# Performance work log

Hardware: AMD Instinct MI355X
Metric: run time of the kernel (lower is better)

The kernel has to match this reference:

```python
import jax, jax.numpy as jnp
import numpy as np

N = 400000
IN, H, F, S, OUT = 64, 256, 128, 16, 5


def setup_inputs() -> dict:
    key = jax.random.key(0)
    ks = jax.random.split(key, 20)
    def lin(k, fan_in, fan_out):
        bound = 1.0 / np.sqrt(fan_in)
        kw, kb = jax.random.split(k)
        W = jax.random.uniform(kw, (fan_in, fan_out), jnp.float32, -bound, bound)
        b = jax.random.uniform(kb, (fan_out,), jnp.float32, -bound, bound)
        return W, b
    pw1, pb1 = lin(ks[0], IN, H)
    pw2, pb2 = lin(ks[1], H, H)
    pw3, pb3 = lin(ks[2], H, F)
    rw1, rb1 = lin(ks[3], F, H)
    rw2, rb2 = lin(ks[4], H, H)
    rw3, rb3 = lin(ks[5], H, F)
    w1, b1 = lin(ks[6], F + S, H)
    w2, b2 = lin(ks[7], H, H)
    w3, b3 = lin(ks[8], H, OUT)
    x = jax.random.normal(ks[9], (N, IN), jnp.float32)
    x_static = jax.random.normal(ks[10], (S,), jnp.float32)
    return {
        "x": x, "x_static": x_static,
        "pw1": pw1, "pb1": pb1, "pw2": pw2, "pb2": pb2, "pw3": pw3, "pb3": pb3,
        "rw1": rw1, "rb1": rb1, "rw2": rw2, "rb2": rb2, "rw3": rw3, "rb3": rb3,
        "w1": w1, "b1": b1, "w2": w2, "b2": b2, "w3": w3, "b3": b3,
    }


def reference(x, x_static, pw1, pb1, pw2, pb2, pw3, pb3,
              rw1, rb1, rw2, rb2, rw3, rb3, w1, b1, w2, b2, w3, b3):
    # phi network applied to every row, then sum-pool (DeepSets).
    # Batched matmuls replace the original Python per-row loop; the per-row
    # bias of the final phi Linear is summed N times, matching the loop.
    h = jax.nn.relu(x @ pw1 + pb1)              # [N, H]
    h = jax.nn.relu(h @ pw2 + pb2)              # [N, H]
    phi = h @ pw3 + pb3                          # [N, F]
    fp = jnp.sum(phi, axis=0)                    # [F]
    # rho network
    r = jax.nn.relu(fp @ rw1 + rb1)
    r = jax.nn.relu(r @ rw2 + rb2)
    r = r @ rw3 + rb3                            # [F]
    out = jnp.concatenate([r, x_static], axis=0)  # [F + S]
    out = jax.nn.relu(out @ w1 + b1)
    out = jax.nn.relu(out @ w2 + b2)
    return out @ w3 + b3                          # [OUT]
```

## Files before the change

kernel.cpp:

```cpp
#include <hip/hip_runtime.h>


typedef unsigned short u16;
typedef _Float16 f16x8 __attribute__((ext_vector_type(8)));
typedef _Float16 f16x4v __attribute__((ext_vector_type(4)));
typedef float f32x4 __attribute__((ext_vector_type(4)));
typedef int i32x4 __attribute__((ext_vector_type(4)));

#define NBLK 256

#define OPW3 0
#define ORW1 32768
#define ORW2 65536
#define ORW3 131072
#define OHW1 163840
#define OHW2 200704
#define OHW3 266240
#define NTW  267520

__global__ void prep_kernel(const float* __restrict__ pw1, const float* __restrict__ pw2,
                            _Float16* __restrict__ w1f, _Float16* __restrict__ w2f,
                            float* __restrict__ gsum, _Float16* __restrict__ tw,
                            const float* __restrict__ pw3, const float* __restrict__ rw1,
                            const float* __restrict__ rw2, const float* __restrict__ rw3,
                            const float* __restrict__ hw1, const float* __restrict__ hw2,
                            const float* __restrict__ hw3) {
    int idx = blockIdx.x * blockDim.x + threadIdx.x;
    if (idx < 256) gsum[idx] = 0.f;
    if (idx < 16384) {
        int j = idx & 7, l = (idx >> 3) & 63, ks = (idx >> 9) & 1, ct = idx >> 10;
        int k = 32 * ks + 8 * (l >> 4) + j;
        int col = 16 * ct + (l & 15);
        w1f[idx] = (_Float16)pw1[k * 256 + col];
    } else {
        int o = idx - 16384;
        int j = o & 7, l = (o >> 3) & 63, ks = (o >> 9) & 7, ct = o >> 12;
        int k = 32 * ks + 8 * (l >> 4) + j;
        int col = 16 * ct + (l & 15);
        w2f[o] = (_Float16)pw2[k * 256 + col];
    }
    if (idx < NTW / 4) {
        int r = idx * 4;
        const float* src;
        if (r < ORW1)      src = pw3 + r;
        else if (r < ORW2) src = rw1 + (r - ORW1);
        else if (r < ORW3) src = rw2 + (r - ORW2);
        else if (r < OHW1) src = rw3 + (r - ORW3);
        else if (r < OHW2) src = hw1 + (r - OHW1);
        else if (r < OHW3) src = hw2 + (r - OHW2);
        else               src = hw3 + (r - OHW3);
        float4 v = *(const float4*)src;
        uint2 o;
        o.x = __builtin_bit_cast(unsigned, __builtin_amdgcn_cvt_pkrtz(v.x, v.y));
        o.y = __builtin_bit_cast(unsigned, __builtin_amdgcn_cvt_pkrtz(v.z, v.w));
        *(uint2*)(tw + r) = o;
    }
}

__device__ __forceinline__ void pin_reg(f16x8& v) {
    i32x4 t = __builtin_bit_cast(i32x4, v);
    asm volatile("" : "+v"(t));
    v = __builtin_bit_cast(f16x8, t);
}
__device__ __forceinline__ unsigned pk(float a, float b) {
    return __builtin_bit_cast(unsigned, __builtin_amdgcn_cvt_pkrtz(a, b));
}

__global__ __attribute__((amdgpu_flat_work_group_size(512, 512), amdgpu_waves_per_eu(2, 2)))
void phi_kernel(
    const float* __restrict__ x,
    const float* __restrict__ pb1, const float* __restrict__ pb2,
    const _Float16* __restrict__ w1g, const _Float16* __restrict__ w2g,
    float* __restrict__ gsum, int ntiles) {
    __shared__ __align__(16) u16 xs[2][64 * 64];
    __shared__ __align__(16) u16 h1s[2][64 * 256];

    const int tid = threadIdx.x;
    const int l = tid & 63;
    const int w = tid >> 6;
    const int fr = l & 15;
    const int fg = l >> 4;
    const int wb = w * 32;

    f16x8 w1r[2][2];
#pragma unroll
    for (int ct = 0; ct < 2; ++ct)
#pragma unroll
        for (int ks = 0; ks < 2; ++ks) {
            int ctg = 2 * w + ct;
            w1r[ct][ks] = *(const f16x8*)(w1g + (((ctg << 1) + ks) << 9) + (l << 3));
        }
    f16x8 w2r[2][8];
#pragma unroll
    for (int ct = 0; ct < 2; ++ct)
#pragma unroll
        for (int ks = 0; ks < 8; ++ks) {
            int ctg = 2 * w + ct;
            w2r[ct][ks] = *(const f16x8*)(w2g + (((ctg << 3) + ks) << 9) + (l << 3));
        }
#pragma unroll
    for (int ct = 0; ct < 2; ++ct) {
#pragma unroll
        for (int ks = 0; ks < 2; ++ks) pin_reg(w1r[ct][ks]);
#pragma unroll
        for (int ks = 0; ks < 8; ++ks) pin_reg(w2r[ct][ks]);
    }
    f32x4 b1v[2], b2v[2];
#pragma unroll
    for (int ct = 0; ct < 2; ++ct) {
        int c0 = wb + ct * 16 + fg * 4;
        b1v[ct] = *(const f32x4*)(pb1 + c0);
        b2v[ct] = *(const f32x4*)(pb2 + c0);
    }

    float psum[2][4] = {{0.f, 0.f, 0.f, 0.f}, {0.f, 0.f, 0.f, 0.f}};

    const int t0 = blockIdx.x;
    {
        const float4* xg = (const float4*)(x + (size_t)t0 * 4096);
#pragma unroll
        for (int i = 0; i < 2; ++i) {
            int f4 = tid + i * 512;
            float4 v = xg[f4];
            int row = f4 >> 4, c4 = f4 & 15;
            uint2 o;
            o.x = pk(v.x, v.y);
            o.y = pk(v.z, v.w);
            int byte = (row * 128 + c4 * 8) ^ ((row & 7) << 4);
            *(uint2*)((char*)xs[0] + byte) = o;
        }
    }
    float4 pf0, pf1;
    {
        int tn = (t0 + NBLK < ntiles) ? t0 + NBLK : 0;
        const float4* xg = (const float4*)(x + (size_t)tn * 4096);
        pf0 = xg[tid];
        pf1 = xg[tid + 512];
    }
    __syncthreads();

    int buf = 0, hb = 0;
    for (int t = t0; t < ntiles; t += NBLK) {
#pragma unroll
        for (int i = 0; i < 2; ++i) {
            float4 v = i ? pf1 : pf0;
            int f4 = tid + i * 512;
            int row = f4 >> 4, c4 = f4 & 15;
            uint2 o;
            o.x = pk(v.x, v.y);
            o.y = pk(v.z, v.w);
            int byte = (row * 128 + c4 * 8) ^ ((row & 7) << 4);
            *(uint2*)((char*)xs[buf ^ 1] + byte) = o;
        }
        {
            int tn = (t + 2 * NBLK < ntiles) ? t + 2 * NBLK : 0;
            const float4* xg = (const float4*)(x + (size_t)tn * 4096);
            pf0 = xg[tid];
            pf1 = xg[tid + 512];
        }

        {
            f32x4 acc[2][4] = {};
#pragma unroll
            for (int ks = 0; ks < 2; ++ks) {
                f16x8 bd[4];
#pragma unroll
                for (int rt = 0; rt < 4; ++rt) {
                    int row = (rt << 4) + fr;
                    int byte = ((row << 7) + (ks << 6) + (fg << 4)) ^ ((row & 7) << 4);
                    bd[rt] = *(const f16x8*)((char*)xs[buf] + byte);
                }
#pragma unroll
                for (int ct = 0; ct < 2; ++ct)
#pragma unroll
                    for (int rt = 0; rt < 4; ++rt)
                        acc[ct][rt] = __builtin_amdgcn_mfma_f32_16x16x32_f16(w1r[ct][ks], bd[rt], acc[ct][rt], 0, 0, 0);
            }
#pragma unroll
            for (int ct = 0; ct < 2; ++ct) {
                int c0 = wb + ct * 16 + fg * 4;
#pragma unroll
                for (int rt = 0; rt < 4; ++rt) {
                    int rown = (rt << 4) + fr;
                    uint2 o;
                    o.x = pk(fmaxf(acc[ct][rt][0] + b1v[ct][0], 0.f),
                             fmaxf(acc[ct][rt][1] + b1v[ct][1], 0.f));
                    o.y = pk(fmaxf(acc[ct][rt][2] + b1v[ct][2], 0.f),
                             fmaxf(acc[ct][rt][3] + b1v[ct][3], 0.f));
                    int byte = ((rown << 9) + (c0 << 1)) ^ ((rown & 15) << 4);
                    *(uint2*)((char*)h1s[hb] + byte) = o;
                }
            }
        }
        __syncthreads();

        {
            f32x4 acc2[2][4] = {};
#pragma unroll
            for (int ks = 0; ks < 8; ++ks) {
                f16x8 bd[4];
#pragma unroll
                for (int rt = 0; rt < 4; ++rt) {
                    int row = (rt << 4) + fr;
                    int byte = ((row << 9) + (ks << 6) + (fg << 4)) ^ ((row & 15) << 4);
                    bd[rt] = *(const f16x8*)((char*)h1s[hb] + byte);
                }
#pragma unroll
                for (int ct = 0; ct < 2; ++ct)
#pragma unroll
                    for (int rt = 0; rt < 4; ++rt)
                        acc2[ct][rt] = __builtin_amdgcn_mfma_f32_16x16x32_f16(w2r[ct][ks], bd[rt], acc2[ct][rt], 0, 0, 0);
            }
#pragma unroll
            for (int ct = 0; ct < 2; ++ct)
#pragma unroll
                for (int r = 0; r < 4; ++r) {
                    float v = 0.f;
#pragma unroll
                    for (int rt = 0; rt < 4; ++rt)
                        v += fmaxf(acc2[ct][rt][r] + b2v[ct][r], 0.f);
                    psum[ct][r] += v;
                }
        }
        buf ^= 1;
        hb ^= 1;
    }

#pragma unroll
    for (int ct = 0; ct < 2; ++ct)
#pragma unroll
        for (int r = 0; r < 4; ++r) {
            float v = psum[ct][r];
            v += __shfl_xor(v, 1, 64);
            v += __shfl_xor(v, 2, 64);
            v += __shfl_xor(v, 4, 64);
            v += __shfl_xor(v, 8, 64);
            if (fr == 0) atomicAdd(&gsum[wb + ct * 16 + fg * 4 + r], v);
        }
}

#define LAYER_V4(IN, OUT, OFF, INEXPR, BIASEXPR, OUTARR, DORELU, KQ, KR)       \
    {                                                                          \
        int cg = t & ((OUT) / 4 - 1), q = t / ((OUT) / 4);                     \
        float4 s = make_float4(0.f, 0.f, 0.f, 0.f);                            \
        int i0 = q * (KR);                                                     \
        for (int i = i0; i < i0 + (KR); ++i) {                                 \
            f16x4v wv = *(const f16x4v*)(tw + (OFF) + i * (OUT) + 4 * cg);     \
            float xv = INEXPR;                                                 \
            s.x += xv * (float)wv[0]; s.y += xv * (float)wv[1];                \
            s.z += xv * (float)wv[2]; s.w += xv * (float)wv[3];                \
        }                                                                      \
        *(float4*)&part[q * (OUT) + 4 * cg] = s;                               \
    }                                                                          \
    __syncthreads();                                                           \
    if (t < (OUT)) {                                                           \
        float s = BIASEXPR;                                                    \
        for (int q = 0; q < (KQ); ++q) s += part[q * (OUT) + t];               \
        OUTARR[t] = (DORELU) ? fmaxf(s, 0.f) : s;                              \
    }                                                                          \
    __syncthreads();

__global__ __launch_bounds__(1024) void tail_kernel(
    const float* __restrict__ gsum, const float* __restrict__ xst,
    const _Float16* __restrict__ tw,
    const float* __restrict__ pb3, const float* __restrict__ rb1,
    const float* __restrict__ rb2, const float* __restrict__ rb3,
    const float* __restrict__ hb1, const float* __restrict__ hb2,
    const float* __restrict__ hb3,
    float* __restrict__ out, float nf) {
    __shared__ float fp[128], r1[256], r2[256], tc[144], t1[256], t2[256];
    __shared__ __align__(16) float part[4096];
    const int t = threadIdx.x;

    LAYER_V4(256, 128, OPW3, gsum[i], nf * pb3[t], fp, 0, 32, 8)
    LAYER_V4(128, 256, ORW1, fp[i], rb1[t], r1, 1, 16, 8)
    LAYER_V4(256, 256, ORW2, r1[i], rb2[t], r2, 1, 16, 16)
    LAYER_V4(256, 128, ORW3, r2[i], rb3[t], tc, 0, 32, 8)
    if (t >= 128 && t < 144) tc[t] = xst[t - 128];
    __syncthreads();
    LAYER_V4(144, 256, OHW1, tc[i], hb1[t], t1, 1, 16, 9)
    LAYER_V4(256, 256, OHW2, t1[i], hb2[t], t2, 1, 16, 16)
    {
        int j = t & 255, q = t >> 8, b = 64 * q;
        if (j < 5) {
            float s0 = 0.f, s1 = 0.f;
#pragma unroll
            for (int i = 0; i < 64; i += 2) {
                s0 += t2[b + i]     * (float)tw[OHW3 + (b + i) * 5 + j];
                s1 += t2[b + i + 1] * (float)tw[OHW3 + (b + i + 1) * 5 + j];
            }
            part[q * 8 + j] = s0 + s1;
        }
    }
    __syncthreads();
    if (t < 5) {
        float s = hb3[t];
        for (int q = 0; q < 4; ++q) s += part[q * 8 + t];
        out[t] = s;
    }
}

extern "C" void kernel_launch(void* const* d_in, const int* in_sizes, int n_in,
                              void* d_out, int out_size, void* d_ws, size_t ws_size,
                              hipStream_t stream) {
    (void)n_in; (void)out_size; (void)ws_size;
    const float* x   = (const float*)d_in[0];
    const float* xst = (const float*)d_in[1];
    const float* pw1 = (const float*)d_in[2];
    const float* pb1 = (const float*)d_in[3];
    const float* pw2 = (const float*)d_in[4];
    const float* pb2 = (const float*)d_in[5];
    const float* pw3 = (const float*)d_in[6];
    const float* pb3 = (const float*)d_in[7];
    const float* rw1 = (const float*)d_in[8];
    const float* rb1 = (const float*)d_in[9];
    const float* rw2 = (const float*)d_in[10];
    const float* rb2 = (const float*)d_in[11];
    const float* rw3 = (const float*)d_in[12];
    const float* rb3 = (const float*)d_in[13];
    const float* w1  = (const float*)d_in[14];
    const float* b1  = (const float*)d_in[15];
    const float* w2  = (const float*)d_in[16];
    const float* b2  = (const float*)d_in[17];
    const float* w3  = (const float*)d_in[18];
    const float* b3  = (const float*)d_in[19];
    float* out = (float*)d_out;

    int n = in_sizes[0] / 64;
    int ntiles = n >> 6;

    char* ws = (char*)d_ws;
    float* gsum = (float*)ws;
    _Float16* w1f = (_Float16*)(ws + 2048);
    _Float16* w2f = (_Float16*)(ws + 2048 + 32768);
    _Float16* tw  = (_Float16*)(ws + 2048 + 32768 + 131072);

    prep_kernel<<<160, 512, 0, stream>>>(pw1, pw2, w1f, w2f, gsum, tw,
                                         pw3, rw1, rw2, rw3, w1, w2, w3);
    phi_kernel<<<NBLK, 512, 0, stream>>>(x, pb1, pb2, w1f, w2f, gsum, ntiles);
    tail_kernel<<<1, 1024, 0, stream>>>(gsum, xst, tw, pb3, rb1, rb2, rb3,
                                        b1, b2, b3, out, (float)n);
}
```

Before: 102.1 us.

## Fuse tail MLP into phi kernel via last-block atomic counter

Removes the separate single-block tail kernel launch by having each phi block increment a global counter after its atomic accumulation. The last block to finish runs the rho and head MLP layers itself, reusing the h1s shared buffer as scratch with 512 threads instead of 1024. This saves one kernel launch and its gap, at the cost of thread fences, an extra atomic per block, and a tail computed by half as many threads.

New measurement: 127.4 us. 1.25x slower.

```diff
diff --git a/kernel.cpp b/kernel.cpp
--- a/kernel.cpp
+++ b/kernel.cpp
@@ -26,7 +26,7 @@
                             const float* __restrict__ hw1, const float* __restrict__ hw2,
                             const float* __restrict__ hw3) {
     int idx = blockIdx.x * blockDim.x + threadIdx.x;
-    if (idx < 256) gsum[idx] = 0.f;
+    if (idx < 260) gsum[idx] = 0.f;
     if (idx < 16384) {
         int j = idx & 7, l = (idx >> 3) & 63, ks = (idx >> 9) & 1, ct = idx >> 10;
         int k = 32 * ks + 8 * (l >> 4) + j;
@@ -66,180 +66,7 @@
     return __builtin_bit_cast(unsigned, __builtin_amdgcn_cvt_pkrtz(a, b));
 }
 
-__global__ __attribute__((amdgpu_flat_work_group_size(512, 512), amdgpu_waves_per_eu(2, 2)))
-void phi_kernel(
-    const float* __restrict__ x,
-    const float* __restrict__ pb1, const float* __restrict__ pb2,
-    const _Float16* __restrict__ w1g, const _Float16* __restrict__ w2g,
-    float* __restrict__ gsum, int ntiles) {
-    __shared__ __align__(16) u16 xs[2][64 * 64];
-    __shared__ __align__(16) u16 h1s[2][64 * 256];
-
-    const int tid = threadIdx.x;
-    const int l = tid & 63;
-    const int w = tid >> 6;
-    const int fr = l & 15;
-    const int fg = l >> 4;
-    const int wb = w * 32;
-
-    f16x8 w1r[2][2];
-#pragma unroll
-    for (int ct = 0; ct < 2; ++ct)
-#pragma unroll
-        for (int ks = 0; ks < 2; ++ks) {
-            int ctg = 2 * w + ct;
-            w1r[ct][ks] = *(const f16x8*)(w1g + (((ctg << 1) + ks) << 9) + (l << 3));
-        }
-    f16x8 w2r[2][8];
-#pragma unroll
-    for (int ct = 0; ct < 2; ++ct)
-#pragma unroll
-        for (int ks = 0; ks < 8; ++ks) {
-            int ctg = 2 * w + ct;
-            w2r[ct][ks] = *(const f16x8*)(w2g + (((ctg << 3) + ks) << 9) + (l << 3));
-        }
-#pragma unroll
-    for (int ct = 0; ct < 2; ++ct) {
-#pragma unroll
-        for (int ks = 0; ks < 2; ++ks) pin_reg(w1r[ct][ks]);
-#pragma unroll
-        for (int ks = 0; ks < 8; ++ks) pin_reg(w2r[ct][ks]);
-    }
-    f32x4 b1v[2], b2v[2];
-#pragma unroll
-    for (int ct = 0; ct < 2; ++ct) {
-        int c0 = wb + ct * 16 + fg * 4;
-        b1v[ct] = *(const f32x4*)(pb1 + c0);
-        b2v[ct] = *(const f32x4*)(pb2 + c0);
-    }
-
-    float psum[2][4] = {{0.f, 0.f, 0.f, 0.f}, {0.f, 0.f, 0.f, 0.f}};
-
-    const int t0 = blockIdx.x;
-    {
-        const float4* xg = (const float4*)(x + (size_t)t0 * 4096);
-#pragma unroll
-        for (int i = 0; i < 2; ++i) {
-            int f4 = tid + i * 512;
-            float4 v = xg[f4];
-            int row = f4 >> 4, c4 = f4 & 15;
-            uint2 o;
-            o.x = pk(v.x, v.y);
-            o.y = pk(v.z, v.w);
-            int byte = (row * 128 + c4 * 8) ^ ((row & 7) << 4);
-            *(uint2*)((char*)xs[0] + byte) = o;
-        }
-    }
-    float4 pf0, pf1;
-    {
-        int tn = (t0 + NBLK < ntiles) ? t0 + NBLK : 0;
-        const float4* xg = (const float4*)(x + (size_t)tn * 4096);
-        pf0 = xg[tid];
-        pf1 = xg[tid + 512];
-    }
-    __syncthreads();
-
-    int buf = 0, hb = 0;
-    for (int t = t0; t < ntiles; t += NBLK) {
-#pragma unroll
-        for (int i = 0; i < 2; ++i) {
-            float4 v = i ? pf1 : pf0;
-            int f4 = tid + i * 512;
-            int row = f4 >> 4, c4 = f4 & 15;
-            uint2 o;
-            o.x = pk(v.x, v.y);
-            o.y = pk(v.z, v.w);
-            int byte = (row * 128 + c4 * 8) ^ ((row & 7) << 4);
-            *(uint2*)((char*)xs[buf ^ 1] + byte) = o;
-        }
-        {
-            int tn = (t + 2 * NBLK < ntiles) ? t + 2 * NBLK : 0;
-            const float4* xg = (const float4*)(x + (size_t)tn * 4096);
-            pf0 = xg[tid];
-            pf1 = xg[tid + 512];
-        }
-
-        {
-            f32x4 acc[2][4] = {};
-#pragma unroll
-            for (int ks = 0; ks < 2; ++ks) {
-                f16x8 bd[4];
-#pragma unroll
-                for (int rt = 0; rt < 4; ++rt) {
-                    int row = (rt << 4) + fr;
-                    int byte = ((row << 7) + (ks << 6) + (fg << 4)) ^ ((row & 7) << 4);
-                    bd[rt] = *(const f16x8*)((char*)xs[buf] + byte);
-                }
-#pragma unroll
-                for (int ct = 0; ct < 2; ++ct)
-#pragma unroll
-                    for (int rt = 0; rt < 4; ++rt)
-                        acc[ct][rt] = __builtin_amdgcn_mfma_f32_16x16x32_f16(w1r[ct][ks], bd[rt], acc[ct][rt], 0, 0, 0);
-            }
-#pragma unroll
-            for (int ct = 0; ct < 2; ++ct) {
-                int c0 = wb + ct * 16 + fg * 4;
-#pragma unroll
-                for (int rt = 0; rt < 4; ++rt) {
-                    int rown = (rt << 4) + fr;
-                    uint2 o;
-                    o.x = pk(fmaxf(acc[ct][rt][0] + b1v[ct][0], 0.f),
-                             fmaxf(acc[ct][rt][1] + b1v[ct][1], 0.f));
-                    o.y = pk(fmaxf(acc[ct][rt][2] + b1v[ct][2], 0.f),
-                             fmaxf(acc[ct][rt][3] + b1v[ct][3], 0.f));
-                    int byte = ((rown << 9) + (c0 << 1)) ^ ((rown & 15) << 4);
-                    *(uint2*)((char*)h1s[hb] + byte) = o;
-                }
-            }
-        }
-        __syncthreads();
-
-        {
-            f32x4 acc2[2][4] = {};
-#pragma unroll
-            for (int ks = 0; ks < 8; ++ks) {
-                f16x8 bd[4];
-#pragma unroll
-                for (int rt = 0; rt < 4; ++rt) {
-                    int row = (rt << 4) + fr;
-                    int byte = ((row << 9) + (ks << 6) + (fg << 4)) ^ ((row & 15) << 4);
-                    bd[rt] = *(const f16x8*)((char*)h1s[hb] + byte);
-                }
-#pragma unroll
-                for (int ct = 0; ct < 2; ++ct)
-#pragma unroll
-                    for (int rt = 0; rt < 4; ++rt)
-                        acc2[ct][rt] = __builtin_amdgcn_mfma_f32_16x16x32_f16(w2r[ct][ks], bd[rt], acc2[ct][rt], 0, 0, 0);
-            }
-#pragma unroll
-            for (int ct = 0; ct < 2; ++ct)
-#pragma unroll
-                for (int r = 0; r < 4; ++r) {
-                    float v = 0.f;
-#pragma unroll
-                    for (int rt = 0; rt < 4; ++rt)
-                        v += fmaxf(acc2[ct][rt][r] + b2v[ct][r], 0.f);
-                    psum[ct][r] += v;
-                }
-        }
-        buf ^= 1;
-        hb ^= 1;
-    }
-
-#pragma unroll
-    for (int ct = 0; ct < 2; ++ct)
-#pragma unroll
-        for (int r = 0; r < 4; ++r) {
-            float v = psum[ct][r];
-            v += __shfl_xor(v, 1, 64);
-            v += __shfl_xor(v, 2, 64);
-            v += __shfl_xor(v, 4, 64);
-            v += __shfl_xor(v, 8, 64);
-            if (fr == 0) atomicAdd(&gsum[wb + ct * 16 + fg * 4 + r], v);
-        }
-}
-
-#define LAYER_V4(IN, OUT, OFF, INEXPR, BIASEXPR, OUTARR, DORELU, KQ, KR)       \
+#define LAYER_V4(OUT, OFF, INEXPR, BIASEXPR, OUTARR, DORELU, KQ, KR)           \
     {                                                                          \
         int cg = t & ((OUT) / 4 - 1), q = t / ((OUT) / 4);                     \
         float4 s = make_float4(0.f, 0.f, 0.f, 0.f);                            \
@@ -260,44 +87,226 @@
     }                                                                          \
     __syncthreads();
 
-__global__ __launch_bounds__(1024) void tail_kernel(
-    const float* __restrict__ gsum, const float* __restrict__ xst,
-    const _Float16* __restrict__ tw,
+__global__ __attribute__((amdgpu_flat_work_group_size(512, 512), amdgpu_waves_per_eu(2, 2)))
+void phi_kernel(
+    const float* __restrict__ x,
+    const float* __restrict__ pb1, const float* __restrict__ pb2,
+    const _Float16* __restrict__ w1g, const _Float16* __restrict__ w2g,
+    float* __restrict__ gsum, int ntiles,
+    const float* __restrict__ xst, const _Float16* __restrict__ tw,
     const float* __restrict__ pb3, const float* __restrict__ rb1,
     const float* __restrict__ rb2, const float* __restrict__ rb3,
     const float* __restrict__ hb1, const float* __restrict__ hb2,
     const float* __restrict__ hb3,
-    float* __restrict__ out, float nf) {
-    __shared__ float fp[128], r1[256], r2[256], tc[144], t1[256], t2[256];
-    __shared__ __align__(16) float part[4096];
-    const int t = threadIdx.x;
-
-    LAYER_V4(256, 128, OPW3, gsum[i], nf * pb3[t], fp, 0, 32, 8)
-    LAYER_V4(128, 256, ORW1, fp[i], rb1[t], r1, 1, 16, 8)
-    LAYER_V4(256, 256, ORW2, r1[i], rb2[t], r2, 1, 16, 16)
-    LAYER_V4(256, 128, ORW3, r2[i], rb3[t], tc, 0, 32, 8)
-    if (t >= 128 && t < 144) tc[t] = xst[t - 128];
-    __syncthreads();
-    LAYER_V4(144, 256, OHW1, tc[i], hb1[t], t1, 1, 16, 9)
-    LAYER_V4(256, 256, OHW2, t1[i], hb2[t], t2, 1, 16, 16)
+    float* __restrict__ outp, float nf) {
+    __shared__ __align__(16) u16 xs[2][64 * 64];
+    __shared__ __align__(16) u16 h1s[2][64 * 256];
+    __shared__ int lastflag;
+
+    const int tid = threadIdx.x;
+    const int l = tid & 63;
+    const int w = tid >> 6;
+    const int fr = l & 15;
+    const int fg = l >> 4;
+    const int wb = w * 32;
+
+    f16x8 w1r[2][2];
+#pragma unroll
+    for (int ct = 0; ct < 2; ++ct)
+#pragma unroll
+        for (int ks = 0; ks < 2; ++ks) {
+            int ctg = 2 * w + ct;
+            w1r[ct][ks] = *(const f16x8*)(w1g + (((ctg << 1) + ks) << 9) + (l << 3));
+        }
+    f16x8 w2r[2][8];
+#pragma unroll
+    for (int ct = 0; ct < 2; ++ct)
+#pragma unroll
+        for (int ks = 0; ks < 8; ++ks) {
+            int ctg = 2 * w + ct;
+            w2r[ct][ks] = *(const f16x8*)(w2g + (((ctg << 3) + ks) << 9) + (l << 3));
+        }
+#pragma unroll
+    for (int ct = 0; ct < 2; ++ct) {
+#pragma unroll
+        for (int ks = 0; ks < 2; ++ks) pin_reg(w1r[ct][ks]);
+#pragma unroll
+        for (int ks = 0; ks < 8; ++ks) pin_reg(w2r[ct][ks]);
+    }
+    f32x4 b1v[2], b2v[2];
+#pragma unroll
+    for (int ct = 0; ct < 2; ++ct) {
+        int c0 = wb + ct * 16 + fg * 4;
+        b1v[ct] = *(const f32x4*)(pb1 + c0);
+        b2v[ct] = *(const f32x4*)(pb2 + c0);
+    }
+
+    float psum[2][4] = {{0.f, 0.f, 0.f, 0.f}, {0.f, 0.f, 0.f, 0.f}};
+
+    const int t0 = blockIdx.x;
     {
-        int j = t & 255, q = t >> 8, b = 64 * q;
+        const float4* xg = (const float4*)(x + (size_t)t0 * 4096);
+#pragma unroll
+        for (int i = 0; i < 2; ++i) {
+            int f4 = tid + i * 512;
+            float4 v = xg[f4];
+            int row = f4 >> 4, c4 = f4 & 15;
+            uint2 o;
+            o.x = pk(v.x, v.y);
+            o.y = pk(v.z, v.w);
+            int byte = (row * 128 + c4 * 8) ^ ((row & 7) << 4);
+            *(uint2*)((char*)xs[0] + byte) = o;
+        }
+    }
+    float4 pf0, pf1;
+    {
+        int tn = (t0 + NBLK < ntiles) ? t0 + NBLK : 0;
+        const float4* xg = (const float4*)(x + (size_t)tn * 4096);
+        pf0 = xg[tid];
+        pf1 = xg[tid + 512];
+    }
+    __syncthreads();
+
+    int buf = 0, hb = 0;
+    for (int t = t0; t < ntiles; t += NBLK) {
+#pragma unroll
+        for (int i = 0; i < 2; ++i) {
+            float4 v = i ? pf1 : pf0;
+            int f4 = tid + i * 512;
+            int row = f4 >> 4, c4 = f4 & 15;
+            uint2 o;
+            o.x = pk(v.x, v.y);
+            o.y = pk(v.z, v.w);
+            int byte = (row * 128 + c4 * 8) ^ ((row & 7) << 4);
+            *(uint2*)((char*)xs[buf ^ 1] + byte) = o;
+        }
+        {
+            int tn = (t + 2 * NBLK < ntiles) ? t + 2 * NBLK : 0;
+            const float4* xg = (const float4*)(x + (size_t)tn * 4096);
+            pf0 = xg[tid];
+            pf1 = xg[tid + 512];
+        }
+
+        {
+            f32x4 acc[2][4] = {};
+#pragma unroll
+            for (int ks = 0; ks < 2; ++ks) {
+                f16x8 bd[4];
+#pragma unroll
+                for (int rt = 0; rt < 4; ++rt) {
+                    int row = (rt << 4) + fr;
+                    int byte = ((row << 7) + (ks << 6) + (fg << 4)) ^ ((row & 7) << 4);
+                    bd[rt] = *(const f16x8*)((char*)xs[buf] + byte);
+                }
+#pragma unroll
+                for (int ct = 0; ct < 2; ++ct)
+#pragma unroll
+                    for (int rt = 0; rt < 4; ++rt)
+                        acc[ct][rt] = __builtin_amdgcn_mfma_f32_16x16x32_f16(w1r[ct][ks], bd[rt], acc[ct][rt], 0, 0, 0);
+            }
+#pragma unroll
+            for (int ct = 0; ct < 2; ++ct) {
+                int c0 = wb + ct * 16 + fg * 4;
+#pragma unroll
+                for (int rt = 0; rt < 4; ++rt) {
+                    int rown = (rt << 4) + fr;
+                    uint2 o;
+                    o.x = pk(fmaxf(acc[ct][rt][0] + b1v[ct][0], 0.f),
+                             fmaxf(acc[ct][rt][1] + b1v[ct][1], 0.f));
+                    o.y = pk(fmaxf(acc[ct][rt][2] + b1v[ct][2], 0.f),
+                             fmaxf(acc[ct][rt][3] + b1v[ct][3], 0.f));
+                    int byte = ((rown << 9) + (c0 << 1)) ^ ((rown & 15) << 4);
+                    *(uint2*)((char*)h1s[hb] + byte) = o;
+                }
+            }
+        }
+        __syncthreads();
+
+        {
+            f32x4 acc2[2][4] = {};
+#pragma unroll
+            for (int ks = 0; ks < 8; ++ks) {
+                f16x8 bd[4];
+#pragma unroll
+                for (int rt = 0; rt < 4; ++rt) {
+                    int row = (rt << 4) + fr;
+                    int byte = ((row << 9) + (ks << 6) + (fg << 4)) ^ ((row & 15) << 4);
+                    bd[rt] = *(const f16x8*)((char*)h1s[hb] + byte);
+                }
+#pragma unroll
+                for (int ct = 0; ct < 2; ++ct)
+#pragma unroll
+                    for (int rt = 0; rt < 4; ++rt)
+                        acc2[ct][rt] = __builtin_amdgcn_mfma_f32_16x16x32_f16(w2r[ct][ks], bd[rt], acc2[ct][rt], 0, 0, 0);
+            }
+#pragma unroll
+            for (int ct = 0; ct < 2; ++ct)
+#pragma unroll
+                for (int r = 0; r < 4; ++r) {
+                    float v = 0.f;
+#pragma unroll
+                    for (int rt = 0; rt < 4; ++rt)
+                        v += fmaxf(acc2[ct][rt][r] + b2v[ct][r], 0.f);
+                    psum[ct][r] += v;
+                }
+        }
+        buf ^= 1;
+        hb ^= 1;
+    }
+
+#pragma unroll
+    for (int ct = 0; ct < 2; ++ct)
+#pragma unroll
+        for (int r = 0; r < 4; ++r) {
+            float v = psum[ct][r];
+            v += __shfl_xor(v, 1, 64);
+            v += __shfl_xor(v, 2, 64);
+            v += __shfl_xor(v, 4, 64);
+            v += __shfl_xor(v, 8, 64);
+            if (fr == 0) atomicAdd(&gsum[wb + ct * 16 + fg * 4 + r], v);
+        }
+
+    __threadfence();
+    if (tid == 0) {
+        int old = atomicAdd((int*)(gsum + 256), 1);
+        lastflag = (old == NBLK - 1);
+    }
+    __syncthreads();
+    if (!lastflag) return;
+    __threadfence();
+
+    float* sb  = (float*)h1s;
+    float* fp  = sb;
+    float* r1v = sb + 128;
+    float* r2v = sb + 384;
+    float* tcv = sb + 640;
+    float* t1v = sb + 784;
+    float* t2v = sb + 1040;
+    float* part = sb + 1296;
+    const int t = tid;
+
+    LAYER_V4(128, OPW3, gsum[i], nf * pb3[t], fp, 0, 16, 16)
+    LAYER_V4(256, ORW1, fp[i], rb1[t], r1v, 1, 8, 16)
+    LAYER_V4(256, ORW2, r1v[i], rb2[t], r2v, 1, 8, 32)
+    LAYER_V4(128, ORW3, r2v[i], rb3[t], tcv, 0, 16, 16)
+    if (t >= 128 && t < 144) tcv[t] = xst[t - 128];
+    __syncthreads();
+    LAYER_V4(256, OHW1, tcv[i], hb1[t], t1v, 1, 8, 18)
+    LAYER_V4(256, OHW2, t1v[i], hb2[t], t2v, 1, 8, 32)
+    {
+        int j = t & 255, q = t >> 8, b = 128 * q;
         if (j < 5) {
             float s0 = 0.f, s1 = 0.f;
 #pragma unroll
-            for (int i = 0; i < 64; i += 2) {
-                s0 += t2[b + i]     * (float)tw[OHW3 + (b + i) * 5 + j];
-                s1 += t2[b + i + 1] * (float)tw[OHW3 + (b + i + 1) * 5 + j];
+            for (int i = 0; i < 128; i += 2) {
+                s0 += t2v[b + i]     * (float)tw[OHW3 + (b + i) * 5 + j];
+                s1 += t2v[b + i + 1] * (float)tw[OHW3 + (b + i + 1) * 5 + j];
             }
             part[q * 8 + j] = s0 + s1;
         }
     }
     __syncthreads();
-    if (t < 5) {
-        float s = hb3[t];
-        for (int q = 0; q < 4; ++q) s += part[q * 8 + t];
-        out[t] = s;
-    }
+    if (t < 5) outp[t] = hb3[t] + part[t] + part[8 + t];
 }
 
 extern "C" void kernel_launch(void* const* d_in, const int* in_sizes, int n_in,
@@ -337,7 +346,7 @@
 
     prep_kernel<<<160, 512, 0, stream>>>(pw1, pw2, w1f, w2f, gsum, tw,
                                          pw3, rw1, rw2, rw3, w1, w2, w3);
-    phi_kernel<<<NBLK, 512, 0, stream>>>(x, pb1, pb2, w1f, w2f, gsum, ntiles);
-    tail_kernel<<<1, 1024, 0, stream>>>(gsum, xst, tw, pb3, rb1, rb2, rb3,
-                                        b1, b2, b3, out, (float)n);
-}
+    phi_kernel<<<NBLK, 512, 0, stream>>>(x, pb1, pb2, w1f, w2f, gsum, ntiles,
+                                         xst, tw, pb3, rb1, rb2, rb3,
+                                         b1, b2, b3, out, (float)n);
+}
```
